# Kernel tuning notes

Measured on AMD Instinct MI355X. Metric: run time of the kernel, lower is better.

## Reference

```python
import jax, jax.numpy as jnp
import numpy as np

B, L, E, H, DV, V = 256, 512, 200, 256, 30000, 50000
NEG_INF = -jnp.inf

def setup_inputs() -> dict:
    key = jax.random.key(0)
    ks = jax.random.split(key, 16)
    s = 0.05
    f = jnp.float32
    return {
        "input_id": jax.random.randint(ks[0], (B, 1), 0, V),
        "input_emb": jax.random.normal(ks[1], (B, 1, E), f),
        "encoder_outputs": jax.random.normal(ks[2], (B, L, H), f),
        "encoder_input_ids": jax.random.randint(ks[3], (B, L), 0, V),
        "hidden": jax.random.normal(ks[4], (B, 1, H), f),
        "attention": jax.random.normal(ks[5], (B, 1, H), f),
        # GRU (PyTorch layout): W_ih (3H, 2H+E), W_hh (3H, H), gate order r,z,n
        "W_ih": jax.random.normal(ks[6], (3 * H, 2 * H + E), f) * s,
        "W_hh": jax.random.normal(ks[7], (3 * H, H), f) * s,
        "b_ih": jnp.zeros((3 * H,), f),
        "b_hh": jnp.zeros((3 * H,), f),
        "W_attn": jax.random.normal(ks[8], (H, H), f) * s,
        "b_attn": jnp.zeros((H,), f),
        "W_comb": jax.random.normal(ks[9], (H, 2 * H), f) * s,
        "b_comb": jnp.zeros((H,), f),
        "W_gen": jax.random.normal(ks[10], (DV, H), f) * s,
        "b_gen": jnp.zeros((DV,), f),
        "W_copy": jax.random.normal(ks[11], (H, H), f) * s,
        "b_copy": jnp.zeros((H,), f),
    }


def reference(input_id, input_emb, encoder_outputs, encoder_input_ids, hidden,
              attention, W_ih, W_hh, b_ih, b_hh, W_attn, b_attn, W_comb,
              b_comb, W_gen, b_gen, W_copy, b_copy):
    b, l = encoder_input_ids.shape
    # selective read: rou = normalized match mask (NaN guard -> 0)
    mask = (input_id == encoder_input_ids).astype(encoder_outputs.dtype)  # (b,l)
    msum = jnp.sum(mask, axis=1, keepdims=True)
    rou = jnp.where(msum > 0, mask / jnp.where(msum > 0, msum, 1.0), 0.0)
    selective_read = jnp.einsum('bl,blh->bh', rou, encoder_outputs)  # (b,h)

    # GRU single step (dropout is identity at inference)
    x = jnp.concatenate([input_emb[:, 0], attention[:, 0], selective_read], axis=-1)
    h_prev = hidden[:, 0]  # (b,h)
    gx = x @ W_ih.T + b_ih          # (b,3h)
    gh = h_prev @ W_hh.T + b_hh     # (b,3h)
    xr, xz, xn = jnp.split(gx, 3, axis=-1)
    hr, hz, hn = jnp.split(gh, 3, axis=-1)
    r = jax.nn.sigmoid(xr + hr)
    z = jax.nn.sigmoid(xz + hz)
    n = jnp.tanh(xn + r * hn)
    h = (1.0 - z) * n + z * h_prev  # (b,h) cur_hidden

    # attention
    q = h @ W_attn.T + b_attn
    attn_w = jax.nn.softmax(jnp.einsum('bh,blh->bl', q, encoder_outputs), axis=-1)
    attn_applied = jnp.einsum('bl,blh->bh', attn_w, encoder_outputs)
    cur_attention = jnp.tanh(
        jnp.concatenate([attn_applied, h], axis=-1) @ W_comb.T + b_comb)  # (b,h)

    # generate + copy scores, joint softmax
    generate_score = cur_attention @ W_gen.T + b_gen                     # (b,DV)
    copy_weights = jax.nn.sigmoid(encoder_outputs @ W_copy.T + b_copy)   # (b,l,h)
    copy_score = jnp.einsum('blh,bh->bl', copy_weights, cur_attention)   # (b,l)
    score = jax.nn.softmax(jnp.concatenate([generate_score, copy_score], axis=1), axis=1)
    gen_s, copy_s = score[:, :DV], score[:, DV:]

    # fused equivalent of the one-hot scatter/mix: direct scatter-add into vocab
    output = jnp.zeros((b, V), score.dtype)
    output = output.at[:, :DV].add(gen_s)
    output = output.at[jnp.arange(b)[:, None], encoder_input_ids].add(copy_s)

    pos = output > 0
    out = jnp.where(pos, jnp.log(jnp.where(pos, output, 1.0)), NEG_INF)
    return out, h[:, None, :], cur_attention[:, None, :]
```

## Files before the change

kernel.cpp:

```cpp
#include <hip/hip_runtime.h>
#include <cmath>

#define B_  256
#define L_  512
#define E_  200
#define H_  256
#define DV_ 30000
#define V_  50000
#define X_  712
#define G3_ 768

#define NEG_BIG -1.0e30f

typedef __attribute__((ext_vector_type(8))) _Float16 half8;
typedef __attribute__((ext_vector_type(4))) float   floatx4;

#define GLOAD16(gptr, lptr)                                                            \
    __builtin_amdgcn_global_load_lds(                                                  \
        (const __attribute__((address_space(1))) unsigned int*)(gptr),                 \
        (__attribute__((address_space(3))) unsigned int*)(lptr), 16, 0, 0)

__global__ void k_cast_wc(const float* __restrict__ Wc, _Float16* __restrict__ wcb) {
    int i = blockIdx.x * 256 + threadIdx.x;
    wcb[i] = (_Float16)Wc[i];
}

__global__ void k_selread(const int* __restrict__ input_id, const float* __restrict__ emb,
                          const float* __restrict__ attention, const float* __restrict__ hidden,
                          const float* __restrict__ enc, const int* __restrict__ enc_ids,
                          float* __restrict__ xT) {
    int b = blockIdx.x, t = threadIdx.x;
    __shared__ int cnt;
    __shared__ int list[L_];
    if (t == 0) cnt = 0;
    __syncthreads();
    int id = input_id[b];
    for (int l = t; l < L_; l += 256) {
        if (enc_ids[b * L_ + l] == id) { int p = atomicAdd(&cnt, 1); list[p] = l; }
    }
    __syncthreads();
    int n = cnt;
    float s = 0.f;
    for (int i = 0; i < n; i++) s += enc[(b * L_ + list[i]) * H_ + t];
    float sel = (n > 0) ? s / (float)n : 0.f;
    for (int k = t; k < E_; k += 256) xT[k * B_ + b] = emb[b * E_ + k];
    xT[(E_ + t) * B_ + b]       = attention[b * H_ + t];
    xT[(E_ + H_ + t) * B_ + b]  = sel;
    xT[(X_ + t) * B_ + b]       = hidden[b * H_ + t];
}

template<int K, int OS>
__global__ void __launch_bounds__(256) k_gru_one(const float* __restrict__ xTp, const float* __restrict__ W,
                                                 const float* __restrict__ bias, float* __restrict__ g) {
    __shared__ __align__(16) float Ws[8 * K];
    int t  = threadIdx.x;
    int j0 = blockIdx.x * 8;
    int bq = t & 63;
    int jh = t >> 6;
#pragma unroll
    for (int jj = 0; jj < 8; jj++) {
        const float4* src = (const float4*)(W + (size_t)(j0 + jj) * K);
        float4* dst = (float4*)(Ws + jj * K);
        for (int i = t; i < K / 4; i += 256) dst[i] = src[i];
    }
    __syncthreads();
    float acc0[4] = {0.f, 0.f, 0.f, 0.f};
    float acc1[4] = {0.f, 0.f, 0.f, 0.f};
    const float* w0 = Ws + (jh * 2 + 0) * K;
    const float* w1 = Ws + (jh * 2 + 1) * K;
#pragma unroll 2
    for (int k4 = 0; k4 < K / 4; k4++) {
        float4 wa = *(const float4*)(w0 + k4 * 4);
        float4 wb = *(const float4*)(w1 + k4 * 4);
        float wav[4] = {wa.x, wa.y, wa.z, wa.w};
        float wbv[4] = {wb.x, wb.y, wb.z, wb.w};
#pragma unroll
        for (int u = 0; u < 4; u++) {
            float4 xv = *(const float4*)(xTp + (size_t)(k4 * 4 + u) * B_ + bq * 4);
            acc0[0] += wav[u] * xv.x; acc0[1] += wav[u] * xv.y;
            acc0[2] += wav[u] * xv.z; acc0[3] += wav[u] * xv.w;
            acc1[0] += wbv[u] * xv.x; acc1[1] += wbv[u] * xv.y;
            acc1[2] += wbv[u] * xv.z; acc1[3] += wbv[u] * xv.w;
        }
    }
    int ja = j0 + jh * 2, jb = ja + 1;
    float ba = bias[ja], bb = bias[jb];
#pragma unroll
    for (int i = 0; i < 4; i++) {
        g[(size_t)(bq * 4 + i) * OS + ja] = acc0[i] + ba;
        g[(size_t)(bq * 4 + i) * OS + jb] = acc1[i] + bb;
    }
}

__global__ void k_gru_gates(const float* __restrict__ gx, const float* __restrict__ gh,
                            const float* __restrict__ hidden, float* __restrict__ hws,
                            float* __restrict__ hT, float* __restrict__ hout) {
    int b = blockIdx.x, j = threadIdx.x;
    float xr = gx[b * G3_ + j], xz = gx[b * G3_ + 256 + j], xn = gx[b * G3_ + 512 + j];
    float hr = gh[b * G3_ + j], hz = gh[b * G3_ + 256 + j], hn = gh[b * G3_ + 512 + j];
    float r = 1.f / (1.f + expf(-(xr + hr)));
    float z = 1.f / (1.f + expf(-(xz + hz)));
    float n = tanhf(xn + r * hn);
    float hp = hidden[b * H_ + j];
    float h = (1.f - z) * n + z * hp;
    hws[b * H_ + j] = h;
    hT[j * B_ + b]  = h;
    hout[b * H_ + j] = h;
}

#define NC_ 4
#define CR_ 128
__global__ void __launch_bounds__(256) k_attn_a(const float* __restrict__ qws, const float* __restrict__ enc,
                         float* __restrict__ avp, float* __restrict__ mdp) {
    int blk = blockIdx.x;
    int b = blk >> 2, c = blk & 3;
    int t = threadIdx.x, lane = t & 63, w = t >> 6;
    __shared__ float ps[CR_];
    __shared__ float red[8];
    const float* encc = enc + ((size_t)b * L_ + c * CR_) * H_;
    float4 q4 = *(const float4*)&qws[b * H_ + lane * 4];
    for (int i = 0; i < 32; i += 8) {
        float s[8];
#pragma unroll
        for (int u = 0; u < 8; u++) {
            float4 e = *(const float4*)(encc + (size_t)(w * 32 + i + u) * H_ + lane * 4);
            s[u] = q4.x * e.x + q4.y * e.y + q4.z * e.z + q4.w * e.w;
        }
#pragma unroll
        for (int u = 0; u < 8; u++) {
#pragma unroll
            for (int o = 1; o < 64; o <<= 1) s[u] += __shfl_xor(s[u], o);
            if (lane == 0) ps[w * 32 + i + u] = s[u];
        }
    }
    __syncthreads();
    {
        float v = ps[w * 32 + (lane & 31)];
#pragma unroll
        for (int o = 1; o < 64; o <<= 1) v = fmaxf(v, __shfl_xor(v, o));
        if (lane == 0) red[w] = v;
    }
    __syncthreads();
    float M = fmaxf(fmaxf(red[0], red[1]), fmaxf(red[2], red[3]));
    float e = (t < CR_) ? __expf(ps[t] - M) : 0.f;
    {
        float ssum = e;
#pragma unroll
        for (int o = 1; o < 64; o <<= 1) ssum += __shfl_xor(ssum, o);
        if (lane == 0) red[4 + w] = ssum;
    }
    __syncthreads();
    if (t < CR_) ps[t] = e;
    if (t == 0) {
        mdp[blk * 2]     = M;
        mdp[blk * 2 + 1] = red[4] + red[5] + red[6] + red[7];
    }
    __syncthreads();
    float a0 = 0.f, a1 = 0.f, a2 = 0.f, a3 = 0.f;
#pragma unroll 4
    for (int r = 0; r < CR_; r += 4) {
        a0 += ps[r + 0] * encc[(size_t)(r + 0) * H_ + t];
        a1 += ps[r + 1] * encc[(size_t)(r + 1) * H_ + t];
        a2 += ps[r + 2] * encc[(size_t)(r + 2) * H_ + t];
        a3 += ps[r + 3] * encc[(size_t)(r + 3) * H_ + t];
    }
    avp[(size_t)blk * H_ + t] = (a0 + a1) + (a2 + a3);
}

__global__ void __launch_bounds__(256) k_attn_b(const float* __restrict__ avp, const float* __restrict__ mdp,
                         const float* __restrict__ hws, const float* __restrict__ W_comb,
                         const float* __restrict__ b_comb,
                         float* __restrict__ caws, _Float16* __restrict__ cab,
                         float* __restrict__ caout) {
    int b = blockIdx.x, t = threadIdx.x;
    __shared__ __align__(16) float xs[2 * H_];
    float m0 = mdp[(b * 4 + 0) * 2], d0 = mdp[(b * 4 + 0) * 2 + 1];
    float m1 = mdp[(b * 4 + 1) * 2], d1 = mdp[(b * 4 + 1) * 2 + 1];
    float m2 = mdp[(b * 4 + 2) * 2], d2 = mdp[(b * 4 + 2) * 2 + 1];
    float m3 = mdp[(b * 4 + 3) * 2], d3 = mdp[(b * 4 + 3) * 2 + 1];
    float M = fmaxf(fmaxf(m0, m1), fmaxf(m2, m3));
    float f0 = __expf(m0 - M), f1 = __expf(m1 - M), f2 = __expf(m2 - M), f3 = __expf(m3 - M);
    float den = f0 * d0 + f1 * d1 + f2 * d2 + f3 * d3;
    float num = f0 * avp[((size_t)b * 4 + 0) * H_ + t] + f1 * avp[((size_t)b * 4 + 1) * H_ + t]
              + f2 * avp[((size_t)b * 4 + 2) * H_ + t] + f3 * avp[((size_t)b * 4 + 3) * H_ + t];
    xs[t]      = num / den;
    xs[H_ + t] = hws[b * H_ + t];
    __syncthreads();
    const float4* wr = (const float4*)(W_comb + (size_t)t * (2 * H_));
    const float4* xp = (const float4*)xs;
    float acc = 0.f;
#pragma unroll 8
    for (int k4 = 0; k4 < 128; k4++) {
        float4 wv = wr[k4], xv = xp[k4];
        acc += wv.x * xv.x + wv.y * xv.y + wv.z * xv.z + wv.w * xv.w;
    }
    float cav = tanhf(b_comb[t] + acc);
    caws[b * H_ + t]  = cav;
    cab[b * H_ + t]   = (_Float16)cav;
    caout[b * H_ + t] = cav;
}

__global__ void __launch_bounds__(256, 2) k_gen_mfma(
        const _Float16* __restrict__ cab, const float* __restrict__ W_gen,
        const float* __restrict__ b_gen, float* __restrict__ out) {
    __shared__ __align__(16) _Float16 Ah[128 * 32];
    __shared__ __align__(16) float    Bf[128 * 32];
    int t = threadIdx.x, w = t >> 6, lane = t & 63;
    int n0 = blockIdx.x * 128, m0 = blockIdx.y * 128;
    int wm = (w >> 1) * 64, wn = (w & 1) * 64;
    int l15 = lane & 15, q = lane >> 4;
    floatx4 acc[4][4];
#pragma unroll
    for (int i = 0; i < 4; i++)
#pragma unroll
        for (int j = 0; j < 4; j++) acc[i][j] = (floatx4){0.f, 0.f, 0.f, 0.f};

    for (int kc = 0; kc < H_; kc += 32) {
#pragma unroll
        for (int i = 0; i < 2; i++) {
            int t2 = w * 2 + i;
            int row = t2 * 16 + (lane >> 2);
            const _Float16* g = cab + (size_t)(m0 + row) * H_ + kc + (lane & 3) * 8;
            GLOAD16(g, &Ah[t2 * 512]);
        }
#pragma unroll
        for (int i = 0; i < 4; i++) {
            int t2 = w * 4 + i;
            int row = t2 * 8 + (lane >> 3);
            int nn = n0 + row; nn = nn < DV_ ? nn : DV_ - 1;
            const float* g = W_gen + (size_t)nn * H_ + kc + (lane & 7) * 4;
            GLOAD16(g, &Bf[t2 * 256]);
        }
        __syncthreads();
        half8 a[4];
#pragma unroll
        for (int mi = 0; mi < 4; mi++) {
            int m = wm + mi * 16 + l15;
            a[mi] = *(const half8*)&Ah[m * 32 + q * 8];
        }
#pragma unroll
        for (int ni = 0; ni < 4; ni++) {
            int n = wn + ni * 16 + l15;
            const float4* bp = (const float4*)&Bf[n * 32 + q * 8];
            float4 f0 = bp[0], f1 = bp[1];
            half8 bf;
            bf[0] = (_Float16)f0.x; bf[1] = (_Float16)f0.y; bf[2] = (_Float16)f0.z; bf[3] = (_Float16)f0.w;
            bf[4] = (_Float16)f1.x; bf[5] = (_Float16)f1.y; bf[6] = (_Float16)f1.z; bf[7] = (_Float16)f1.w;
#pragma unroll
            for (int mi = 0; mi < 4; mi++)
                acc[mi][ni] = __builtin_amdgcn_mfma_f32_16x16x32_f16(a[mi], bf, acc[mi][ni], 0, 0, 0);
        }
        __syncthreads();
    }
#pragma unroll
    for (int ni = 0; ni < 4; ni++) {
        int col = n0 + wn + ni * 16 + l15;
        if (col < DV_) {
            float bg = b_gen[col];
#pragma unroll
            for (int mi = 0; mi < 4; mi++)
#pragma unroll
                for (int j = 0; j < 4; j++) {
                    int row = m0 + wm + mi * 16 + q * 4 + j;
                    out[(size_t)row * V_ + col] = acc[mi][ni][j] + bg;
                }
        }
    }
}

__global__ void __launch_bounds__(256, 2) k_copy_mfma(
        const float* __restrict__ enc, const _Float16* __restrict__ wcb,
        const float* __restrict__ b_copy, const float* __restrict__ caws,
        float* __restrict__ copy_s) {
    __shared__ __align__(16) float    Af[128 * 32];
    __shared__ __align__(16) _Float16 Bh[256 * 32];
    __shared__ float bcs[H_], cas[H_];
    int t = threadIdx.x, w = t >> 6, lane = t & 63;
    int R0 = blockIdx.x * 128;
    int b  = blockIdx.x >> 2;
    int l15 = lane & 15, q = lane >> 4;
    bcs[t] = b_copy[t];
    cas[t] = caws[b * H_ + t];
    floatx4 acc[2][16];
#pragma unroll
    for (int i = 0; i < 2; i++)
#pragma unroll
        for (int j = 0; j < 16; j++) acc[i][j] = (floatx4){0.f, 0.f, 0.f, 0.f};

    for (int kc = 0; kc < H_; kc += 32) {
#pragma unroll
        for (int i = 0; i < 4; i++) {
            int t2 = w * 4 + i;
            int row = t2 * 8 + (lane >> 3);
            const float* g = enc + (size_t)(R0 + row) * H_ + kc + (lane & 7) * 4;
            GLOAD16(g, &Af[t2 * 256]);
        }
#pragma unroll
        for (int i = 0; i < 4; i++) {
            int t2 = w * 4 + i;
            int row = t2 * 16 + (lane >> 2);
            const _Float16* g = wcb + row * H_ + kc + (lane & 3) * 8;
            GLOAD16(g, &Bh[t2 * 512]);
        }
        __syncthreads();
        half8 a[2];
#pragma unroll
        for (int mi = 0; mi < 2; mi++) {
            int m = w * 32 + mi * 16 + l15;
            const float4* apx = (const float4*)&Af[m * 32 + q * 8];
            float4 f0 = apx[0], f1 = apx[1];
            half8 h;
            h[0] = (_Float16)f0.x; h[1] = (_Float16)f0.y; h[2] = (_Float16)f0.z; h[3] = (_Float16)f0.w;
            h[4] = (_Float16)f1.x; h[5] = (_Float16)f1.y; h[6] = (_Float16)f1.z; h[7] = (_Float16)f1.w;
            a[mi] = h;
        }
#pragma unroll
        for (int ni = 0; ni < 16; ni++) {
            int n = ni * 16 + l15;
            half8 bf = *(const half8*)&Bh[n * 32 + q * 8];
            acc[0][ni] = __builtin_amdgcn_mfma_f32_16x16x32_f16(a[0], bf, acc[0][ni], 0, 0, 0);
            acc[1][ni] = __builtin_amdgcn_mfma_f32_16x16x32_f16(a[1], bf, acc[1][ni], 0, 0, 0);
        }
        __syncthreads();
    }
#pragma unroll
    for (int mi = 0; mi < 2; mi++) {
#pragma unroll
        for (int j = 0; j < 4; j++) {
            float p = 0.f;
#pragma unroll
            for (int ni = 0; ni < 16; ni++) {
                int col = ni * 16 + l15;
                float v = acc[mi][ni][j] + bcs[col];
                p += cas[col] / (1.f + __expf(-v));
            }
            p += __shfl_xor(p, 1);
            p += __shfl_xor(p, 2);
            p += __shfl_xor(p, 4);
            p += __shfl_xor(p, 8);
            if (l15 == 0) copy_s[R0 + w * 32 + mi * 16 + q * 4 + j] = p;
        }
    }
}

__global__ void __launch_bounds__(1024) k_stats(const float* __restrict__ out, const float* __restrict__ copy_s,
                        float* __restrict__ mrow, float* __restrict__ ldrow) {
    int b = blockIdx.x, t = threadIdx.x, lane = t & 63, w = t >> 6;
    __shared__ float rm[16], rs[16];
    const float* row = out + (size_t)b * V_;
    float m = -INFINITY, s = 0.f;
    for (int j = t; j < DV_; j += 1024) {
        float v = row[j];
        if (v > m) { s = s * __expf(m - v) + 1.f; m = v; }
        else       s += __expf(v - m);
    }
    if (t < 512) {
        float v = copy_s[b * L_ + t];
        if (v > m) { s = s * __expf(m - v) + 1.f; m = v; }
        else       s += __expf(v - m);
    }
#pragma unroll
    for (int o = 1; o < 64; o <<= 1) {
        float m2 = __shfl_xor(m, o), s2 = __shfl_xor(s, o);
        float mn = fmaxf(m, m2);
        s = s * __expf(m - mn) + s2 * __expf(m2 - mn);
        m = mn;
    }
    if (lane == 0) { rm[w] = m; rs[w] = s; }
    __syncthreads();
    if (t == 0) {
        float M = rm[0], S = rs[0];
        for (int i = 1; i < 16; i++) {
            float mn = fmaxf(M, rm[i]);
            S = S * __expf(M - mn) + rs[i] * __expf(rm[i] - mn);
            M = mn;
        }
        mrow[b] = M;
        ldrow[b] = __logf(S);
    }
}

__global__ void __launch_bounds__(1024) k_final(float* __restrict__ out, const float* __restrict__ mrow,
                        const float* __restrict__ ldrow) {
    int j = blockIdx.x * 1024 + threadIdx.x;
    int b = blockIdx.y;
    if (j >= V_) return;
    size_t idx = (size_t)b * V_ + j;
    float sh = mrow[b] + ldrow[b];
    out[idx] = (j < DV_) ? out[idx] - sh : NEG_BIG;
}

__global__ void k_scatter_log(float* __restrict__ out, const float* __restrict__ copy_s,
                              const int* __restrict__ enc_ids, const float* __restrict__ mrow,
                              const float* __restrict__ ldrow) {
    int l = blockIdx.x * 256 + threadIdx.x;
    int b = blockIdx.y;
    float p = __expf(copy_s[b * L_ + l] - mrow[b] - ldrow[b]);
    unsigned int* up = (unsigned int*)(out + (size_t)b * V_ + enc_ids[b * L_ + l]);
    unsigned int cur = *up;
    while (true) {
        float ov = __uint_as_float(cur);
        float pv = (ov < -1.0e29f) ? p : __expf(ov) + p;
        unsigned int prev = atomicCAS(up, cur, __float_as_uint(__logf(pv)));
        if (prev == cur) break;
        cur = prev;
    }
}

extern "C" void kernel_launch(void* const* d_in, const int* in_sizes, int n_in,
                              void* d_out, int out_size, void* d_ws, size_t ws_size,
                              hipStream_t stream) {
    const int*   input_id  = (const int*)  d_in[0];
    const float* input_emb = (const float*)d_in[1];
    const float* enc       = (const float*)d_in[2];
    const int*   enc_ids   = (const int*)  d_in[3];
    const float* hidden    = (const float*)d_in[4];
    const float* attention = (const float*)d_in[5];
    const float* W_ih      = (const float*)d_in[6];
    const float* W_hh      = (const float*)d_in[7];
    const float* b_ih      = (const float*)d_in[8];
    const float* b_hh      = (const float*)d_in[9];
    const float* W_attn    = (const float*)d_in[10];
    const float* b_attn    = (const float*)d_in[11];
    const float* W_comb    = (const float*)d_in[12];
    const float* b_comb    = (const float*)d_in[13];
    const float* W_gen     = (const float*)d_in[14];
    const float* b_gen     = (const float*)d_in[15];
    const float* W_copy    = (const float*)d_in[16];
    const float* b_copy    = (const float*)d_in[17];

    float* out = (float*)d_out;
    float* ws  = (float*)d_ws;
    float* xT   = ws;
    float* gx   = xT + 247808;
    float* gh   = gx + 196608;
    float* hws  = gh + 196608;
    float* caws = hws + 65536;
    float* cps  = caws + 65536;
    float* mrow = cps + 131072;
    float* ldrow = mrow + 256;
    _Float16* wcb = (_Float16*)(ldrow + 256);
    _Float16* cab = wcb + 65536;
    float* qws  = (float*)(cab + 65536);
    float* mdp  = qws + 65536;
    float* hT   = xT;
    float* avp  = gx;

    float* hout  = out + (size_t)B_ * V_;
    float* caout = hout + B_ * H_;

    k_cast_wc<<<256, 256, 0, stream>>>(W_copy, wcb);
    k_selread<<<256, 256, 0, stream>>>(input_id, input_emb, attention, hidden, enc, enc_ids, xT);
    k_gru_one<712, G3_><<<96, 256, 0, stream>>>(xT, W_ih, b_ih, gx);
    k_gru_one<256, G3_><<<96, 256, 0, stream>>>(xT + X_ * B_, W_hh, b_hh, gh);
    k_gru_gates<<<256, 256, 0, stream>>>(gx, gh, hidden, hws, hT, hout);
    k_gru_one<256, H_><<<32, 256, 0, stream>>>(hT, W_attn, b_attn, qws);
    k_attn_a<<<B_ * NC_, 256, 0, stream>>>(qws, enc, avp, mdp);
    k_attn_b<<<256, 256, 0, stream>>>(avp, mdp, hws, W_comb, b_comb, caws, cab, caout);
    k_gen_mfma<<<dim3((DV_ + 127) / 128, 2), 256, 0, stream>>>(cab, W_gen, b_gen, out);
    k_copy_mfma<<<(B_ * L_) / 128, 256, 0, stream>>>(enc, wcb, b_copy, caws, cps);
    k_stats<<<256, 1024, 0, stream>>>(out, cps, mrow, ldrow);
    dim3 gf((V_ + 1023) / 1024, B_);
    k_final<<<gf, 1024, 0, stream>>>(out, mrow, ldrow);
    dim3 gs(L_ / 256, B_);
    k_scatter_log<<<gs, 256, 0, stream>>>(out, cps, enc_ids, mrow, ldrow);
}
```

Measured before the change: 487.5 us.

## Fuse per-tile softmax stats into generate GEMM epilogue and vectorize final pass

The generate GEMM epilogue now computes per-row running max and sum-exp for each 128-column tile and writes them to a partials buffer. The stats kernel merges these 235 partials with the copy scores instead of re-reading the full 30000-wide logits row. The final normalization pass uses float4 loads and stores, and the W_copy fp16 cast is folded into the selective-read kernel to save a launch. The cost is extra exp and shuffle work plus a block barrier in the GEMM epilogue.

```diff
diff --git a/kernel.cpp b/kernel.cpp
--- a/kernel.cpp
+++ b/kernel.cpp
@@ -9,6 +9,7 @@
 #define V_  50000
 #define X_  712
 #define G3_ 768
+#define NT_ 235
 
 #define NEG_BIG -1.0e30f
 
@@ -20,20 +21,17 @@
         (const __attribute__((address_space(1))) unsigned int*)(gptr),                 \
         (__attribute__((address_space(3))) unsigned int*)(lptr), 16, 0, 0)
 
-__global__ void k_cast_wc(const float* __restrict__ Wc, _Float16* __restrict__ wcb) {
-    int i = blockIdx.x * 256 + threadIdx.x;
-    wcb[i] = (_Float16)Wc[i];
-}
-
 __global__ void k_selread(const int* __restrict__ input_id, const float* __restrict__ emb,
                           const float* __restrict__ attention, const float* __restrict__ hidden,
                           const float* __restrict__ enc, const int* __restrict__ enc_ids,
+                          const float* __restrict__ Wc, _Float16* __restrict__ wcb,
                           float* __restrict__ xT) {
     int b = blockIdx.x, t = threadIdx.x;
     __shared__ int cnt;
     __shared__ int list[L_];
     if (t == 0) cnt = 0;
     __syncthreads();
+    wcb[b * H_ + t] = (_Float16)Wc[b * H_ + t];
     int id = input_id[b];
     for (int l = t; l < L_; l += 256) {
         if (enc_ids[b * L_ + l] == id) { int p = atomicAdd(&cnt, 1); list[p] = l; }
@@ -202,9 +200,11 @@
 
 __global__ void __launch_bounds__(256, 2) k_gen_mfma(
         const _Float16* __restrict__ cab, const float* __restrict__ W_gen,
-        const float* __restrict__ b_gen, float* __restrict__ out) {
+        const float* __restrict__ b_gen, float* __restrict__ out,
+        float2* __restrict__ pmd) {
     __shared__ __align__(16) _Float16 Ah[128 * 32];
     __shared__ __align__(16) float    Bf[128 * 32];
+    __shared__ float mm[4][128], dd[4][128];
     int t = threadIdx.x, w = t >> 6, lane = t & 63;
     int n0 = blockIdx.x * 128, m0 = blockIdx.y * 128;
     int wm = (w >> 1) * 64, wn = (w & 1) * 64;
@@ -252,11 +252,13 @@
         }
         __syncthreads();
     }
+    float bgs[4];
 #pragma unroll
     for (int ni = 0; ni < 4; ni++) {
         int col = n0 + wn + ni * 16 + l15;
         if (col < DV_) {
             float bg = b_gen[col];
+            bgs[ni] = bg;
 #pragma unroll
             for (int mi = 0; mi < 4; mi++)
 #pragma unroll
@@ -264,7 +266,41 @@
                     int row = m0 + wm + mi * 16 + q * 4 + j;
                     out[(size_t)row * V_ + col] = acc[mi][ni][j] + bg;
                 }
-        }
+        } else bgs[ni] = 0.f;
+    }
+#pragma unroll
+    for (int mi = 0; mi < 4; mi++)
+#pragma unroll
+        for (int j = 0; j < 4; j++) {
+            float m_l = -INFINITY, d_l = 0.f;
+#pragma unroll
+            for (int ni = 0; ni < 4; ni++) {
+                int col = n0 + wn + ni * 16 + l15;
+                float v = (col < DV_) ? acc[mi][ni][j] + bgs[ni] : NEG_BIG;
+                float mn = fmaxf(m_l, v);
+                d_l = d_l * __expf(m_l - mn) + __expf(v - mn);
+                m_l = mn;
+            }
+#pragma unroll
+            for (int o = 1; o < 16; o <<= 1) {
+                float m2 = __shfl_xor(m_l, o), d2 = __shfl_xor(d_l, o);
+                float mn = fmaxf(m_l, m2);
+                d_l = d_l * __expf(m_l - mn) + d2 * __expf(m2 - mn);
+                m_l = mn;
+            }
+            if (l15 == 0) {
+                int rl = wm + mi * 16 + q * 4 + j;
+                mm[w][rl] = m_l; dd[w][rl] = d_l;
+            }
+        }
+    __syncthreads();
+    if (t < 128) {
+        int wa = (t < 64) ? 0 : 2;
+        float ma = mm[wa][t],     da = dd[wa][t];
+        float mb = mm[wa + 1][t], db = dd[wa + 1][t];
+        float M = fmaxf(ma, mb);
+        float D = da * __expf(ma - M) + db * __expf(mb - M);
+        pmd[(size_t)(m0 + t) * NT_ + blockIdx.x] = make_float2(M, D);
     }
 }
 
@@ -343,51 +379,51 @@
     }
 }
 
-__global__ void __launch_bounds__(1024) k_stats(const float* __restrict__ out, const float* __restrict__ copy_s,
-                        float* __restrict__ mrow, float* __restrict__ ldrow) {
+__global__ void __launch_bounds__(256) k_stats2(const float2* __restrict__ pmd, const float* __restrict__ copy_s,
+                         float* __restrict__ mrow, float* __restrict__ ldrow) {
     int b = blockIdx.x, t = threadIdx.x, lane = t & 63, w = t >> 6;
-    __shared__ float rm[16], rs[16];
-    const float* row = out + (size_t)b * V_;
-    float m = -INFINITY, s = 0.f;
-    for (int j = t; j < DV_; j += 1024) {
-        float v = row[j];
-        if (v > m) { s = s * __expf(m - v) + 1.f; m = v; }
-        else       s += __expf(v - m);
-    }
-    if (t < 512) {
-        float v = copy_s[b * L_ + t];
-        if (v > m) { s = s * __expf(m - v) + 1.f; m = v; }
-        else       s += __expf(v - m);
-    }
+    __shared__ float rm[4], rs[4];
+    float m = -INFINITY, d = 0.f;
+    if (t < NT_) { float2 p = pmd[(size_t)b * NT_ + t]; m = p.x; d = p.y; }
+    float v0 = copy_s[b * L_ + t];
+    float v1 = copy_s[b * L_ + 256 + t];
+    float mn = fmaxf(m, v0); d = d * __expf(m - mn) + __expf(v0 - mn); m = mn;
+    mn = fmaxf(m, v1); d = d * __expf(m - mn) + __expf(v1 - mn); m = mn;
 #pragma unroll
     for (int o = 1; o < 64; o <<= 1) {
-        float m2 = __shfl_xor(m, o), s2 = __shfl_xor(s, o);
-        float mn = fmaxf(m, m2);
-        s = s * __expf(m - mn) + s2 * __expf(m2 - mn);
+        float m2 = __shfl_xor(m, o), d2 = __shfl_xor(d, o);
+        mn = fmaxf(m, m2);
+        d = d * __expf(m - mn) + d2 * __expf(m2 - mn);
         m = mn;
     }
-    if (lane == 0) { rm[w] = m; rs[w] = s; }
+    if (lane == 0) { rm[w] = m; rs[w] = d; }
     __syncthreads();
     if (t == 0) {
         float M = rm[0], S = rs[0];
-        for (int i = 1; i < 16; i++) {
-            float mn = fmaxf(M, rm[i]);
-            S = S * __expf(M - mn) + rs[i] * __expf(rm[i] - mn);
-            M = mn;
+        for (int i = 1; i < 4; i++) {
+            float mx = fmaxf(M, rm[i]);
+            S = S * __expf(M - mx) + rs[i] * __expf(rm[i] - mx);
+            M = mx;
         }
         mrow[b] = M;
         ldrow[b] = __logf(S);
     }
 }
 
-__global__ void __launch_bounds__(1024) k_final(float* __restrict__ out, const float* __restrict__ mrow,
+__global__ void __launch_bounds__(256) k_final(float* __restrict__ out, const float* __restrict__ mrow,
                         const float* __restrict__ ldrow) {
-    int j = blockIdx.x * 1024 + threadIdx.x;
+    int idx = blockIdx.x * 256 + threadIdx.x;
     int b = blockIdx.y;
-    if (j >= V_) return;
-    size_t idx = (size_t)b * V_ + j;
+    if (idx >= V_ / 4) return;
+    float4* o4 = (float4*)(out + (size_t)b * V_) + idx;
+    if (idx >= DV_ / 4) {
+        *o4 = make_float4(NEG_BIG, NEG_BIG, NEG_BIG, NEG_BIG);
+        return;
+    }
     float sh = mrow[b] + ldrow[b];
-    out[idx] = (j < DV_) ? out[idx] - sh : NEG_BIG;
+    float4 v = *o4;
+    v.x -= sh; v.y -= sh; v.z -= sh; v.w -= sh;
+    *o4 = v;
 }
 
 __global__ void k_scatter_log(float* __restrict__ out, const float* __restrict__ copy_s,
@@ -443,25 +479,25 @@
     _Float16* cab = wcb + 65536;
     float* qws  = (float*)(cab + 65536);
     float* mdp  = qws + 65536;
+    float2* pmd = (float2*)(mdp + 2048);
     float* hT   = xT;
     float* avp  = gx;
 
     float* hout  = out + (size_t)B_ * V_;
     float* caout = hout + B_ * H_;
 
-    k_cast_wc<<<256, 256, 0, stream>>>(W_copy, wcb);
-    k_selread<<<256, 256, 0, stream>>>(input_id, input_emb, attention, hidden, enc, enc_ids, xT);
+    k_selread<<<256, 256, 0, stream>>>(input_id, input_emb, attention, hidden, enc, enc_ids, W_copy, wcb, xT);
     k_gru_one<712, G3_><<<96, 256, 0, stream>>>(xT, W_ih, b_ih, gx);
     k_gru_one<256, G3_><<<96, 256, 0, stream>>>(xT + X_ * B_, W_hh, b_hh, gh);
     k_gru_gates<<<256, 256, 0, stream>>>(gx, gh, hidden, hws, hT, hout);
     k_gru_one<256, H_><<<32, 256, 0, stream>>>(hT, W_attn, b_attn, qws);
     k_attn_a<<<B_ * NC_, 256, 0, stream>>>(qws, enc, avp, mdp);
     k_attn_b<<<256, 256, 0, stream>>>(avp, mdp, hws, W_comb, b_comb, caws, cab, caout);
-    k_gen_mfma<<<dim3((DV_ + 127) / 128, 2), 256, 0, stream>>>(cab, W_gen, b_gen, out);
+    k_gen_mfma<<<dim3(NT_, 2), 256, 0, stream>>>(cab, W_gen, b_gen, out, pmd);
     k_copy_mfma<<<(B_ * L_) / 128, 256, 0, stream>>>(enc, wcb, b_copy, caws, cps);
-    k_stats<<<256, 1024, 0, stream>>>(out, cps, mrow, ldrow);
-    dim3 gf((V_ + 1023) / 1024, B_);
-    k_final<<<gf, 1024, 0, stream>>>(out, mrow, ldrow);
+    k_stats2<<<256, 256, 0, stream>>>(pmd, cps, mrow, ldrow);
+    dim3 gf((V_ / 4 + 255) / 256, B_);
+    k_final<<<gf, 256, 0, stream>>>(out, mrow, ldrow);
     dim3 gs(L_ / 256, B_);
     k_scatter_log<<<gs, 256, 0, stream>>>(out, cps, enc_ids, mrow, ldrow);
 }
```

Result: no change. 481.2 us (-1.3%).
